# Kernel tuning notes

Hardware: AMD Instinct MI355X
Metric: run time of the kernel (lower is better)

The kernel has to match this reference:

```python
import jax, jax.numpy as jnp
import numpy as np

C_DIM = 640
CTX_DIM = 768
N_HEADS = 8

def setup_inputs() -> dict:
    key = jax.random.key(0)
    ks = jax.random.split(key, 12)
    B, C, H, W = 16, C_DIM, 64, 64
    T = 77
    s_c = 1.0 / np.sqrt(C)
    s_ctx = 1.0 / np.sqrt(CTX_DIM)
    return {
        "x": jax.random.normal(ks[0], (B, C, H, W), jnp.float32),
        "context": jax.random.normal(ks[1], (B, T, CTX_DIM), jnp.float32),
        "Wq": jax.random.normal(ks[2], (C, C), jnp.float32) * s_c,
        "bq": jnp.zeros((C,), jnp.float32),
        "Wk": jax.random.normal(ks[3], (CTX_DIM, C), jnp.float32) * s_ctx,
        "bk": jnp.zeros((C,), jnp.float32),
        "Wv": jax.random.normal(ks[4], (CTX_DIM, C), jnp.float32) * s_ctx,
        "bv": jnp.zeros((C,), jnp.float32),
        "Wo": jax.random.normal(ks[5], (C, C), jnp.float32) * s_c,
        "bo": jnp.zeros((C,), jnp.float32),
    }

def reference(x, context, Wq, bq, Wk, bk, Wv, bv, Wo, bo):
    B, C, H, W = x.shape
    h = N_HEADS
    d = C // h
    scale = d ** (-0.5)
    # (B,C,H,W) -> (B, HW, C)
    xs = x.reshape(B, C, H * W).transpose(0, 2, 1)
    q = xs @ Wq + bq                      # (B, HW, C)
    k = context @ Wk + bk                 # (B, T, C)
    v = context @ Wv + bv                 # (B, T, C)
    q = q.reshape(B, H * W, h, d).transpose(0, 2, 1, 3)  # (B,h,HW,d)
    k = k.reshape(B, -1, h, d).transpose(0, 2, 1, 3)      # (B,h,T,d)
    v = v.reshape(B, -1, h, d).transpose(0, 2, 1, 3)      # (B,h,T,d)
    scores = jnp.einsum('bhnd,bhtd->bhnt', q, k) * scale  # (B,h,HW,T)
    attn = jax.nn.softmax(scores, axis=-1)
    out = jnp.einsum('bhnt,bhtd->bhnd', attn, v)           # (B,h,HW,d)
    out = out.transpose(0, 2, 1, 3).reshape(B, H * W, C)
    out = out @ Wo + bo                                    # (B, HW, C)
    return out.transpose(0, 2, 1).reshape(B, C, H, W)
```

## Files before the change

### kernel.cpp

```cpp
#include <hip/hip_runtime.h>
#include <hip/hip_fp16.h>

typedef _Float16 half_t;
typedef _Float16 f16x8 __attribute__((ext_vector_type(8)));
typedef _Float16 f16x4 __attribute__((ext_vector_type(4)));
typedef float f32x4 __attribute__((ext_vector_type(4)));

#define NB   16
#define CD   640
#define HWD  4096
#define TT   77
#define CTXD 768
#define NH   8
#define DH   80
#define DP   96

#define GLOAD16(gp, lp)                                                        \
  __builtin_amdgcn_global_load_lds(                                            \
      (const __attribute__((address_space(1))) void*)(gp),                     \
      (__attribute__((address_space(3))) void*)(lp), 16, 0, 0)

__device__ inline void xcd_panel_map(int j, int& panel, int& nblk) {
  const int xcd = j & 7, slot = j >> 3;
  panel = (slot / 5) * 8 + xcd;
  nblk = slot % 5;
}

__global__ __launch_bounds__(256) void xpose_kernel(
    const float* __restrict__ x, half_t* __restrict__ xt) {
  __shared__ half_t tile[64][72];
  const float* s = x + (long)blockIdx.z * CD * HWD;
  half_t* d = xt + (long)blockIdx.z * HWD * CD;
  const int r0 = blockIdx.y * 64;
  const int c0 = blockIdx.x * 64;
  const int t = threadIdx.x;
  const int rr = t >> 4, cc = (t & 15) * 4;
#pragma unroll
  for (int j = 0; j < 4; ++j) {
    const int r = rr + j * 16;
    float4 v = *reinterpret_cast<const float4*>(&s[(long)(r0 + r) * HWD + c0 + cc]);
    tile[cc + 0][r] = (half_t)v.x;
    tile[cc + 1][r] = (half_t)v.y;
    tile[cc + 2][r] = (half_t)v.z;
    tile[cc + 3][r] = (half_t)v.w;
  }
  __syncthreads();
  const int cr = t >> 2, rc = (t & 3) * 16;
  half_t* dp = &d[(long)(c0 + cr) * CD + r0 + rc];
  *reinterpret_cast<int4*>(dp)     = *reinterpret_cast<const int4*>(&tile[cr][rc]);
  *reinterpret_cast<int4*>(dp + 8) = *reinterpret_cast<const int4*>(&tile[cr][rc + 8]);
}

__global__ __launch_bounds__(256) void wtrans_kernel(
    const float* __restrict__ Wq, const float* __restrict__ Wk,
    const float* __restrict__ Wv, const float* __restrict__ Wo,
    half_t* __restrict__ WqT, half_t* __restrict__ WkT,
    half_t* __restrict__ WvT, half_t* __restrict__ WoT) {
  __shared__ half_t tile[64][72];
  const int z = blockIdx.z;
  const float* src = (z == 0) ? Wq : (z == 1) ? Wk : (z == 2) ? Wv : Wo;
  half_t* dst      = (z == 0) ? WqT : (z == 1) ? WkT : (z == 2) ? WvT : WoT;
  const int R = (z == 1 || z == 2) ? CTXD : CD;
  const int r0 = blockIdx.y * 64, c0 = blockIdx.x * 64;
  if (r0 >= R) return;
  const int t = threadIdx.x;
  const int rr = t >> 4, cc = (t & 15) * 4;
#pragma unroll
  for (int j = 0; j < 4; ++j) {
    const int r = rr + j * 16;
    float4 v = *reinterpret_cast<const float4*>(&src[(long)(r0 + r) * CD + c0 + cc]);
    tile[cc + 0][r] = (half_t)v.x;
    tile[cc + 1][r] = (half_t)v.y;
    tile[cc + 2][r] = (half_t)v.z;
    tile[cc + 3][r] = (half_t)v.w;
  }
  __syncthreads();
  const int cr = t >> 2, rc = (t & 3) * 16;
  half_t* dp = &dst[(long)(c0 + cr) * R + r0 + rc];
  *reinterpret_cast<int4*>(dp)     = *reinterpret_cast<const int4*>(&tile[cr][rc]);
  *reinterpret_cast<int4*>(dp + 8) = *reinterpret_cast<const int4*>(&tile[cr][rc + 8]);
}

__global__ __launch_bounds__(256) void kv_kernel(
    const float* __restrict__ ctx,
    const half_t* __restrict__ WkT, const half_t* __restrict__ WvT,
    const float* __restrict__ bk, const float* __restrict__ bv,
    half_t* __restrict__ k_ws, half_t* __restrict__ vT_ws) {
  __shared__ half_t C_sm[80][32];
  const int n0 = blockIdx.x * 64;
  const int b  = blockIdx.y;
  const int kv = blockIdx.z;
  const half_t* WT  = kv ? WvT : WkT;
  const float* bias = kv ? bv : bk;
  const int tid = threadIdx.x;
  const int wave = tid >> 6, lane = tid & 63, g = lane >> 4, ln = lane & 15;

  f32x4 acc[5];
#pragma unroll
  for (int i = 0; i < 5; ++i) acc[i] = (f32x4){0.f, 0.f, 0.f, 0.f};

  for (int k0 = 0; k0 < CTXD; k0 += 32) {
    if (k0) __syncthreads();
    for (int i = tid; i < 320; i += 256) {
      const int r = i >> 2, c8 = (i & 3) * 8;
      f16x8 hv = {0, 0, 0, 0, 0, 0, 0, 0};
      if (r < TT) {
        const float* cp = ctx + ((long)b * TT + r) * CTXD + k0 + c8;
        float4 c0v = *reinterpret_cast<const float4*>(cp);
        float4 c1v = *reinterpret_cast<const float4*>(cp + 4);
        hv[0] = (half_t)c0v.x; hv[1] = (half_t)c0v.y;
        hv[2] = (half_t)c0v.z; hv[3] = (half_t)c0v.w;
        hv[4] = (half_t)c1v.x; hv[5] = (half_t)c1v.y;
        hv[6] = (half_t)c1v.z; hv[7] = (half_t)c1v.w;
      }
      *reinterpret_cast<f16x8*>(&C_sm[r][c8]) = hv;
    }
    __syncthreads();
    f16x8 bfr = *reinterpret_cast<const f16x8*>(
        &WT[(long)(n0 + wave * 16 + ln) * CTXD + k0 + g * 8]);
#pragma unroll
    for (int mt = 0; mt < 5; ++mt) {
      f16x8 afr = *reinterpret_cast<const f16x8*>(&C_sm[mt * 16 + ln][g * 8]);
      acc[mt] = __builtin_amdgcn_mfma_f32_16x16x32_f16(afr, bfr, acc[mt], 0, 0, 0);
    }
  }

  const int n = n0 + wave * 16 + ln;
  const float bsv = bias[n];
  const int h = n / DH, dd = n % DH;
  if (kv == 0) {
#pragma unroll
    for (int mt = 0; mt < 5; ++mt)
#pragma unroll
      for (int r = 0; r < 4; ++r) {
        const int t = mt * 16 + g * 4 + r;
        k_ws[(((long)b * NH + h) * 80 + t) * DP + dd] = (half_t)(acc[mt][r] + bsv);
      }
  } else {
#pragma unroll
    for (int mt = 0; mt < 5; ++mt) {
      const int t0 = mt * 16 + g * 4;
      f16x4 v4;
#pragma unroll
      for (int r = 0; r < 4; ++r) v4[r] = (half_t)(acc[mt][r] + bsv);
      *reinterpret_cast<f16x4*>(&vT_ws[(((long)b * NH + h) * 80 + dd) * DP + t0]) = v4;
    }
  }
}

template <int EPI>
__global__ __launch_bounds__(512, 2) void pgemm_kernel(
    const half_t* __restrict__ A, const half_t* __restrict__ BT,
    const float* __restrict__ bias, void* __restrict__ outp) {
  __shared__ half_t A_sm[3][256 * 32];
  __shared__ half_t B_sm[3][128 * 32];
  const int tid = threadIdx.x;
  const int lane = tid & 63, wave = tid >> 6;
  const int g = lane >> 4, ln = lane & 15;
  const int wm = wave >> 1, wn = wave & 1;

  int panel, nblk;
  xcd_panel_map(blockIdx.x, panel, nblk);
  const long m0 = (long)panel * 256;
  const int n0 = nblk * 128;

  const int srow = wave * 16 + (lane >> 2);
  const int sk8 = (((lane & 3) ^ ((lane >> 3) & 3))) * 8;
  const half_t* ag0 = A + (m0 + srow) * CD + sk8;
  const half_t* ag1 = ag0 + 128 * CD;
  const half_t* bg0 = BT + (long)(n0 + srow) * CD + sk8;

  const int rs8 = (g ^ ((ln >> 1) & 3)) * 8;

  f32x4 acc[4][4];
#pragma unroll
  for (int i = 0; i < 4; ++i)
#pragma unroll
    for (int j = 0; j < 4; ++j) acc[i][j] = (f32x4){0.f, 0.f, 0.f, 0.f};

#define STAGE_AB(buf, kt)                                             \
  do {                                                                \
    GLOAD16(ag0 + (long)(kt) * 32, &A_sm[buf][wave * 512]);           \
    GLOAD16(ag1 + (long)(kt) * 32, &A_sm[buf][4096 + wave * 512]);    \
    GLOAD16(bg0 + (long)(kt) * 32, &B_sm[buf][wave * 512]);           \
  } while (0)

  STAGE_AB(0, 0);
  STAGE_AB(1, 1);

  const int nk = CD / 32;
  for (int kt = 0; kt < nk; ++kt) {
    const int cur = kt % 3;
    if (kt + 2 < nk) {
      STAGE_AB((kt + 2) % 3, kt + 2);
      asm volatile("s_waitcnt vmcnt(6)" ::: "memory");
    } else if (kt + 1 < nk) {
      asm volatile("s_waitcnt vmcnt(3)" ::: "memory");
    } else {
      asm volatile("s_waitcnt vmcnt(0)" ::: "memory");
    }
    __builtin_amdgcn_s_barrier();
    __builtin_amdgcn_sched_barrier(0);
    f16x8 af[4], bf[4];
#pragma unroll
    for (int mi = 0; mi < 4; ++mi)
      af[mi] = *reinterpret_cast<const f16x8*>(
          &A_sm[cur][(wm * 64 + mi * 16 + ln) * 32 + rs8]);
#pragma unroll
    for (int ni = 0; ni < 4; ++ni)
      bf[ni] = *reinterpret_cast<const f16x8*>(
          &B_sm[cur][(wn * 64 + ni * 16 + ln) * 32 + rs8]);
    __builtin_amdgcn_s_setprio(1);
#pragma unroll
    for (int mi = 0; mi < 4; ++mi)
#pragma unroll
      for (int ni = 0; ni < 4; ++ni)
        acc[mi][ni] = __builtin_amdgcn_mfma_f32_16x16x32_f16(af[mi], bf[ni], acc[mi][ni], 0, 0, 0);
    __builtin_amdgcn_s_setprio(0);
    __builtin_amdgcn_s_barrier();
  }

  if (EPI == 0) {
    half_t* O = (half_t*)outp;
#pragma unroll
    for (int ni = 0; ni < 4; ++ni) {
      const int n = n0 + wn * 64 + ni * 16 + ln;
      const float bvv = bias[n];
#pragma unroll
      for (int mi = 0; mi < 4; ++mi) {
        const long m = m0 + wm * 64 + mi * 16 + g * 4;
        f32x4 v = acc[mi][ni];
#pragma unroll
        for (int r = 0; r < 4; ++r)
          O[(m + r) * CD + n] = (half_t)(v[r] + bvv);
      }
    }
  } else {
    float* O = (float*)outp;
#pragma unroll
    for (int mi = 0; mi < 4; ++mi) {
      const long m = m0 + wm * 64 + mi * 16 + g * 4;
      const long bb = m >> 12;
      const int p = (int)(m & 4095);
#pragma unroll
      for (int ni = 0; ni < 4; ++ni) {
        const int n = n0 + wn * 64 + ni * 16 + ln;
        const float bvv = bias[n];
        f32x4 v = acc[mi][ni];
        float4 o4 = make_float4(v[0] + bvv, v[1] + bvv, v[2] + bvv, v[3] + bvv);
        *reinterpret_cast<float4*>(&O[((bb * CD + n) << 12) + p]) = o4;
      }
    }
  }
#undef STAGE_AB
}

__global__ __launch_bounds__(512) void attn_kernel(
    const half_t* __restrict__ q_ws, const half_t* __restrict__ k_ws,
    const half_t* __restrict__ vT_ws, half_t* __restrict__ attn_ws) {
  __shared__ half_t K_sm[80][DP];
  __shared__ half_t V_sm[80][DP];
  __shared__ half_t Q_sm[128][DP];
  const int p0 = blockIdx.x * 128;
  const int h  = blockIdx.y;
  const int b  = blockIdx.z;
  const int tid = threadIdx.x, wave = tid >> 6, lane = tid & 63;
  const int g = lane >> 4, ln = lane & 15;

  const half_t* kp = k_ws  + ((long)b * NH + h) * 80 * DP;
  const half_t* vp = vT_ws + ((long)b * NH + h) * 80 * DP;
  for (int i = tid; i < 960; i += 512) {
    reinterpret_cast<int4*>(K_sm)[i] = reinterpret_cast<const int4*>(kp)[i];
    reinterpret_cast<int4*>(V_sm)[i] = reinterpret_cast<const int4*>(vp)[i];
  }
  for (int i = tid; i < 1536; i += 512) {
    const int r = i / 12, c8 = i % 12;
    int4 v = make_int4(0, 0, 0, 0);
    if (c8 < 10)
      v = *reinterpret_cast<const int4*>(
          q_ws + ((long)(b * HWD + p0 + r)) * CD + h * DH + c8 * 8);
    *reinterpret_cast<int4*>(&Q_sm[r][c8 * 8]) = v;
  }
  __syncthreads();

  f32x4 s[5];
#pragma unroll
  for (int i = 0; i < 5; ++i) s[i] = (f32x4){0.f, 0.f, 0.f, 0.f};
#pragma unroll
  for (int ks = 0; ks < 3; ++ks) {
    f16x8 bq = *reinterpret_cast<const f16x8*>(&Q_sm[wave * 16 + ln][ks * 32 + g * 8]);
#pragma unroll
    for (int mt = 0; mt < 5; ++mt) {
      f16x8 ak = *reinterpret_cast<const f16x8*>(&K_sm[mt * 16 + ln][ks * 32 + g * 8]);
      s[mt] = __builtin_amdgcn_mfma_f32_16x16x32_f16(ak, bq, s[mt], 0, 0, 0);
    }
  }

  const float sc = 0.11180339887498949f;
  float mx = -1e30f;
#pragma unroll
  for (int mt = 0; mt < 5; ++mt)
#pragma unroll
    for (int r = 0; r < 4; ++r) {
      const int t = mt * 16 + g * 4 + r;
      const float v = s[mt][r] * sc;
      s[mt][r] = v;
      if (t < TT) mx = fmaxf(mx, v);
    }
  mx = fmaxf(mx, __shfl_xor(mx, 16));
  mx = fmaxf(mx, __shfl_xor(mx, 32));
  float e[5][4];
  float sum = 0.f;
#pragma unroll
  for (int mt = 0; mt < 5; ++mt)
#pragma unroll
    for (int r = 0; r < 4; ++r) {
      const int t = mt * 16 + g * 4 + r;
      float ev = 0.f;
      if (t < TT) { ev = __expf(s[mt][r] - mx); sum += ev; }
      e[mt][r] = ev;
    }
  sum += __shfl_xor(sum, 16);
  sum += __shfl_xor(sum, 32);
  const float inv = 1.f / sum;
#pragma unroll
  for (int mt = 0; mt < 5; ++mt) {
    f16x4 pv;
#pragma unroll
    for (int r = 0; r < 4; ++r) pv[r] = (half_t)(e[mt][r] * inv);
    *reinterpret_cast<f16x4*>(&Q_sm[wave * 16 + ln][mt * 16 + g * 4]) = pv;
  }

  f32x4 o[5];
#pragma unroll
  for (int i = 0; i < 5; ++i) o[i] = (f32x4){0.f, 0.f, 0.f, 0.f};
#pragma unroll
  for (int ks = 0; ks < 3; ++ks) {
    f16x8 bp = *reinterpret_cast<const f16x8*>(&Q_sm[wave * 16 + ln][ks * 32 + g * 8]);
#pragma unroll
    for (int mt = 0; mt < 5; ++mt) {
      f16x8 av = *reinterpret_cast<const f16x8*>(&V_sm[mt * 16 + ln][ks * 32 + g * 8]);
      o[mt] = __builtin_amdgcn_mfma_f32_16x16x32_f16(av, bp, o[mt], 0, 0, 0);
    }
  }

  half_t* op = attn_ws + ((long)(b * HWD + p0 + wave * 16 + ln)) * CD + h * DH;
#pragma unroll
  for (int mt = 0; mt < 5; ++mt) {
    f16x4 v4;
#pragma unroll
    for (int r = 0; r < 4; ++r) v4[r] = (half_t)o[mt][r];
    *reinterpret_cast<f16x4*>(&op[mt * 16 + g * 4]) = v4;
  }
}

extern "C" void kernel_launch(void* const* d_in, const int* in_sizes, int n_in,
                              void* d_out, int out_size, void* d_ws, size_t ws_size,
                              hipStream_t stream) {
  const float* x   = (const float*)d_in[0];
  const float* ctx = (const float*)d_in[1];
  const float* Wq  = (const float*)d_in[2];
  const float* bq  = (const float*)d_in[3];
  const float* Wk  = (const float*)d_in[4];
  const float* bk  = (const float*)d_in[5];
  const float* Wv  = (const float*)d_in[6];
  const float* bv  = (const float*)d_in[7];
  const float* Wo  = (const float*)d_in[8];
  const float* bo  = (const float*)d_in[9];
  float* out = (float*)d_out;

  char* ws = (char*)d_ws;
  size_t off = 0;
  auto alloc = [&](size_t bytes) {
    void* p = ws + off;
    off += (bytes + 255) & ~(size_t)255;
    return p;
  };
  half_t* WqT  = (half_t*)alloc((size_t)CD * CD * 2);
  half_t* WkT  = (half_t*)alloc((size_t)CD * CTXD * 2);
  half_t* WvT  = (half_t*)alloc((size_t)CD * CTXD * 2);
  half_t* WoT  = (half_t*)alloc((size_t)CD * CD * 2);
  half_t* kws  = (half_t*)alloc((size_t)NB * NH * 80 * DP * 2);
  half_t* vTws = (half_t*)alloc((size_t)NB * NH * 80 * DP * 2);
  half_t* xt   = (half_t*)alloc((size_t)NB * HWD * CD * 2);
  half_t* q    = (half_t*)alloc((size_t)NB * HWD * CD * 2);
  half_t* attn = xt;

  hipMemsetAsync(kws, 0, (size_t)2 * NB * NH * 80 * DP * 2, stream);

  wtrans_kernel<<<dim3(CD / 64, CTXD / 64, 4), 256, 0, stream>>>(
      Wq, Wk, Wv, Wo, WqT, WkT, WvT, WoT);

  kv_kernel<<<dim3(CD / 64, NB, 2), 256, 0, stream>>>(ctx, WkT, WvT, bk, bv, kws, vTws);

  xpose_kernel<<<dim3(HWD / 64, CD / 64, NB), 256, 0, stream>>>(x, xt);

  pgemm_kernel<0><<<(CD / 128) * ((NB * HWD) / 256), 512, 0, stream>>>(
      xt, WqT, bq, q);

  attn_kernel<<<dim3(HWD / 128, NH, NB), 512, 0, stream>>>(q, kws, vTws, attn);

  pgemm_kernel<1><<<(CD / 128) * ((NB * HWD) / 256), 512, 0, stream>>>(
      attn, WoT, bo, out);
}
```

Measured before the change: 316.3 us.

## Restructure projection GEMM main loop into interleaved half-tile ping-pong schedule

The projection GEMM's K loop is split into two halves per K-tile. LDS fragment reads and global-to-LDS staging for A and B are interleaved with two groups of 8 MFMAs, separated by barriers and explicit lgkm/vm waits, in the style of a ping-pong schedule. Launch bounds rise to 4 blocks per CU, which pushes register pressure down; the 48KB of LDS per block may still limit occupancy. The aim is better overlap of memory traffic with matrix math, at the cost of extra barriers per iteration and possible register spills.

```diff
diff --git a/kernel.cpp b/kernel.cpp
--- a/kernel.cpp
+++ b/kernel.cpp
@@ -149,11 +149,11 @@
 }
 
 template <int EPI>
-__global__ __launch_bounds__(512, 2) void pgemm_kernel(
+__global__ __launch_bounds__(512, 4) void pgemm8_kernel(
     const half_t* __restrict__ A, const half_t* __restrict__ BT,
     const float* __restrict__ bias, void* __restrict__ outp) {
-  __shared__ half_t A_sm[3][256 * 32];
-  __shared__ half_t B_sm[3][128 * 32];
+  __shared__ __align__(16) half_t A_sm[3][256 * 32];
+  __shared__ __align__(16) half_t B_sm[3][128 * 32];
   const int tid = threadIdx.x;
   const int lane = tid & 63, wave = tid >> 6;
   const int g = lane >> 4, ln = lane & 15;
@@ -164,8 +164,8 @@
   const long m0 = (long)panel * 256;
   const int n0 = nblk * 128;
 
-  const int srow = wave * 16 + (lane >> 2);
-  const int sk8 = (((lane & 3) ^ ((lane >> 3) & 3))) * 8;
+  const int srow = tid >> 2;
+  const int sk8 = ((tid & 3) ^ ((tid >> 3) & 3)) * 8;
   const half_t* ag0 = A + (m0 + srow) * CD + sk8;
   const half_t* ag1 = ag0 + 128 * CD;
   const half_t* bg0 = BT + (long)(n0 + srow) * CD + sk8;
@@ -178,46 +178,97 @@
 #pragma unroll
     for (int j = 0; j < 4; ++j) acc[i][j] = (f32x4){0.f, 0.f, 0.f, 0.f};
 
-#define STAGE_AB(buf, kt)                                             \
+#define STAGE_A(buf, kt)                                              \
   do {                                                                \
     GLOAD16(ag0 + (long)(kt) * 32, &A_sm[buf][wave * 512]);           \
     GLOAD16(ag1 + (long)(kt) * 32, &A_sm[buf][4096 + wave * 512]);    \
-    GLOAD16(bg0 + (long)(kt) * 32, &B_sm[buf][wave * 512]);           \
   } while (0)
-
-  STAGE_AB(0, 0);
-  STAGE_AB(1, 1);
+#define STAGE_B(buf, kt)                                              \
+  GLOAD16(bg0 + (long)(kt) * 32, &B_sm[buf][wave * 512])
+
+#define READ_A2(dst0, dst1, buf, mi0)                                 \
+  do {                                                                \
+    dst0 = *reinterpret_cast<const f16x8*>(                           \
+        &A_sm[buf][(wm * 64 + (mi0) * 16 + ln) * 32 + rs8]);          \
+    dst1 = *reinterpret_cast<const f16x8*>(                           \
+        &A_sm[buf][(wm * 64 + ((mi0) + 1) * 16 + ln) * 32 + rs8]);    \
+  } while (0)
+#define READ_B4(bf, buf)                                              \
+  do {                                                                \
+    _Pragma("unroll")                                                 \
+    for (int ni = 0; ni < 4; ++ni)                                    \
+      bf[ni] = *reinterpret_cast<const f16x8*>(                       \
+          &B_sm[buf][(wn * 64 + ni * 16 + ln) * 32 + rs8]);           \
+  } while (0)
+
+#define MFMA8(a0, a1, bf, mi0)                                        \
+  do {                                                                \
+    __builtin_amdgcn_s_setprio(1);                                    \
+    _Pragma("unroll")                                                 \
+    for (int ni = 0; ni < 4; ++ni)                                    \
+      acc[mi0][ni] = __builtin_amdgcn_mfma_f32_16x16x32_f16(          \
+          a0, bf[ni], acc[mi0][ni], 0, 0, 0);                         \
+    _Pragma("unroll")                                                 \
+    for (int ni = 0; ni < 4; ++ni)                                    \
+      acc[(mi0) + 1][ni] = __builtin_amdgcn_mfma_f32_16x16x32_f16(    \
+          a1, bf[ni], acc[(mi0) + 1][ni], 0, 0, 0);                   \
+    __builtin_amdgcn_s_setprio(0);                                    \
+  } while (0)
+
+#define WAIT_LGKM_FENCE()                                             \
+  do {                                                                \
+    asm volatile("s_waitcnt lgkmcnt(0)" ::: "memory");                \
+    __builtin_amdgcn_sched_barrier(0);                                \
+  } while (0)
+
+  STAGE_A(0, 0); STAGE_B(0, 0);
+  STAGE_A(1, 1); STAGE_B(1, 1);
+  asm volatile("s_waitcnt vmcnt(3)" ::: "memory");
+  __builtin_amdgcn_s_barrier();
 
   const int nk = CD / 32;
-  for (int kt = 0; kt < nk; ++kt) {
-    const int cur = kt % 3;
-    if (kt + 2 < nk) {
-      STAGE_AB((kt + 2) % 3, kt + 2);
-      asm volatile("s_waitcnt vmcnt(6)" ::: "memory");
-    } else if (kt + 1 < nk) {
-      asm volatile("s_waitcnt vmcnt(3)" ::: "memory");
-    } else {
-      asm volatile("s_waitcnt vmcnt(0)" ::: "memory");
-    }
-    __builtin_amdgcn_s_barrier();
-    __builtin_amdgcn_sched_barrier(0);
-    f16x8 af[4], bf[4];
-#pragma unroll
-    for (int mi = 0; mi < 4; ++mi)
-      af[mi] = *reinterpret_cast<const f16x8*>(
-          &A_sm[cur][(wm * 64 + mi * 16 + ln) * 32 + rs8]);
-#pragma unroll
-    for (int ni = 0; ni < 4; ++ni)
-      bf[ni] = *reinterpret_cast<const f16x8*>(
-          &B_sm[cur][(wn * 64 + ni * 16 + ln) * 32 + rs8]);
-    __builtin_amdgcn_s_setprio(1);
-#pragma unroll
-    for (int mi = 0; mi < 4; ++mi)
-#pragma unroll
-      for (int ni = 0; ni < 4; ++ni)
-        acc[mi][ni] = __builtin_amdgcn_mfma_f32_16x16x32_f16(af[mi], bf[ni], acc[mi][ni], 0, 0, 0);
-    __builtin_amdgcn_s_setprio(0);
-    __builtin_amdgcn_s_barrier();
+  f16x8 a0, a1, a2, a3, bf[4];
+  for (int t = 0; t < nk - 2; ++t) {
+    const int cur = t % 3, nxt = (t + 2) % 3;
+    READ_A2(a0, a1, cur, 0);
+    READ_B4(bf, cur);
+    STAGE_A(nxt, t + 2);
+    __builtin_amdgcn_s_barrier();
+    WAIT_LGKM_FENCE();
+    MFMA8(a0, a1, bf, 0);
+    __builtin_amdgcn_s_barrier();
+    READ_A2(a2, a3, cur, 2);
+    STAGE_B(nxt, t + 2);
+    asm volatile("s_waitcnt vmcnt(3)" ::: "memory");
+    __builtin_amdgcn_s_barrier();
+    WAIT_LGKM_FENCE();
+    MFMA8(a2, a3, bf, 2);
+    __builtin_amdgcn_s_barrier();
+  }
+  {
+    const int cur = (nk - 2) % 3;
+    READ_A2(a0, a1, cur, 0);
+    READ_B4(bf, cur);
+    __builtin_amdgcn_s_barrier();
+    WAIT_LGKM_FENCE();
+    MFMA8(a0, a1, bf, 0);
+    __builtin_amdgcn_s_barrier();
+    READ_A2(a2, a3, cur, 2);
+    asm volatile("s_waitcnt vmcnt(0)" ::: "memory");
+    __builtin_amdgcn_s_barrier();
+    WAIT_LGKM_FENCE();
+    MFMA8(a2, a3, bf, 2);
+    __builtin_amdgcn_s_barrier();
+  }
+  {
+    const int cur = (nk - 1) % 3;
+    READ_A2(a0, a1, cur, 0);
+    READ_B4(bf, cur);
+    WAIT_LGKM_FENCE();
+    MFMA8(a0, a1, bf, 0);
+    READ_A2(a2, a3, cur, 2);
+    WAIT_LGKM_FENCE();
+    MFMA8(a2, a3, bf, 2);
   }
 
   if (EPI == 0) {
@@ -252,7 +303,12 @@
       }
     }
   }
-#undef STAGE_AB
+#undef STAGE_A
+#undef STAGE_B
+#undef READ_A2
+#undef READ_B4
+#undef MFMA8
+#undef WAIT_LGKM_FENCE
 }
 
 __global__ __launch_bounds__(512) void attn_kernel(
@@ -395,11 +451,11 @@
 
   xpose_kernel<<<dim3(HWD / 64, CD / 64, NB), 256, 0, stream>>>(x, xt);
 
-  pgemm_kernel<0><<<(CD / 128) * ((NB * HWD) / 256), 512, 0, stream>>>(
+  pgemm8_kernel<0><<<(CD / 128) * ((NB * HWD) / 256), 512, 0, stream>>>(
       xt, WqT, bq, q);
 
   attn_kernel<<<dim3(HWD / 128, NH, NB), 512, 0, stream>>>(q, kws, vTws, attn);
 
-  pgemm_kernel<1><<<(CD / 128) * ((NB * HWD) / 256), 512, 0, stream>>>(
+  pgemm8_kernel<1><<<(CD / 128) * ((NB * HWD) / 256), 512, 0, stream>>>(
       attn, WoT, bo, out);
 }
```

Result: no change. 311.1 us (-1.6%).
